# Performance work log

Measured on AMD Instinct MI355X. Metric: run time of the kernel, lower is better.

Reference implementation:

```python
import jax, jax.numpy as jnp
import numpy as np

B, T, EMB, H = 4, 2048, 1024, 16
S = EMB // H


def setup_inputs() -> dict:
    key = jax.random.key(0)
    ks = jax.random.split(key, 7)
    x = jax.random.normal(ks[0], (B, T, EMB), dtype=jnp.float32)
    pad_amounts = jax.random.randint(ks[1], (B,), 0, 512, dtype=jnp.int64)
    Wk = jax.random.normal(ks[2], (S, S), dtype=jnp.float32) * (1.0 / np.sqrt(S))
    Wq = jax.random.normal(ks[3], (S, S), dtype=jnp.float32) * (1.0 / np.sqrt(S))
    Wv = jax.random.normal(ks[4], (S, S), dtype=jnp.float32) * (1.0 / np.sqrt(S))
    Wu = jax.random.normal(ks[5], (EMB, EMB), dtype=jnp.float32) * (1.0 / np.sqrt(EMB))
    bu = jax.random.normal(ks[6], (EMB,), dtype=jnp.float32) * 0.01
    return {"x": x, "Wk": Wk, "Wq": Wq, "Wv": Wv, "Wu": Wu, "bu": bu,
            "pad_amounts": pad_amounts}


def reference(x, Wk, Wq, Wv, Wu, bu, pad_amounts):
    b, t, e = x.shape
    h = H
    s = e // h
    xh = x.reshape(b, t, h, s)
    # torch Linear: y = x @ W.T (no bias for k/q/v)
    keys = jnp.einsum('bths,os->btho', xh, Wk)
    queries = jnp.einsum('bths,os->btho', xh, Wq)
    values = jnp.einsum('bths,os->btho', xh, Wv)
    # (b,t,h,s) -> (b*h,t,s)
    keys = keys.transpose(0, 2, 1, 3).reshape(b * h, t, s)
    queries = queries.transpose(0, 2, 1, 3).reshape(b * h, t, s)
    values = values.transpose(0, 2, 1, 3).reshape(b * h, t, s)
    scale = e ** 0.25
    queries = queries / scale
    keys = keys / scale
    dot = jnp.einsum('nqs,nks->nqk', queries, keys)  # (b*h, t, t)
    # Faithful to original bug: only the first b flat indices of b*h get masked.
    pad_full = jnp.concatenate([pad_amounts,
                                jnp.zeros(b * h - b, dtype=pad_amounts.dtype)])
    thresh = (t - pad_full)[:, None, None]  # (b*h,1,1); thresh=t -> no mask
    pos = jnp.arange(t)
    mask = (pos[None, :, None] >= thresh) & (pos[None, None, :] >= thresh)
    dot = jnp.where(mask, -jnp.inf, dot)
    att = jax.nn.softmax(dot, axis=2)
    out = jnp.einsum('nqk,nks->nqs', att, values)  # (b*h,t,s)
    out = out.reshape(b, h, t, s).transpose(0, 2, 1, 3).reshape(b, t, h * s)
    return out @ Wu.T + bu
```

## Files before the change

### kernel.cpp

```cpp
#include <hip/hip_runtime.h>


typedef float f32x4 __attribute__((ext_vector_type(4)));
typedef float f32x16 __attribute__((ext_vector_type(16)));
typedef __bf16 bf16x8 __attribute__((ext_vector_type(8)));
typedef unsigned u32x4 __attribute__((ext_vector_type(4)));

#define MFMA16(a, b, c) __builtin_amdgcn_mfma_f32_16x16x32_bf16((a), (b), (c), 0, 0, 0)
#define MFMA32(a, b, c) __builtin_amdgcn_mfma_f32_32x32x16_bf16((a), (b), (c), 0, 0, 0)

constexpr int Tn = 2048;
constexpr int Bn = 4;
constexpr int EMBn = 1024;
constexpr float NEG_INF = -3.0e38f;

__device__ __forceinline__ float exp2_hw(float x) {
  float r; asm("v_exp_f32 %0, %1" : "=v"(r) : "v"(x)); return r;
}
__device__ __forceinline__ unsigned cvtpk(float lo, float hi) {
  unsigned r; asm("v_cvt_pk_bf16_f32 %0, %1, %2" : "=v"(r) : "v"(lo), "v"(hi)); return r;
}
__device__ __forceinline__ void permswap(unsigned& a, unsigned& b) {
  asm("v_permlane32_swap_b32 %0, %1" : "+v"(a), "+v"(b));
}

__global__ __launch_bounds__(256) void sa_prep(
    const float* __restrict__ Wk, const float* __restrict__ Wq,
    const float* __restrict__ Wv, const float* __restrict__ Wu,
    __bf16* __restrict__ w3, __bf16* __restrict__ wub) {
  int idx = blockIdx.x * 256 + threadIdx.x;
  const float rs = 0.21233046f;
  if (idx < 1048576) wub[idx] = (__bf16)Wu[idx];
  if (idx < 4096) {
    w3[idx]        = (__bf16)(Wk[idx] * rs);
    w3[4096 + idx] = (__bf16)(Wq[idx] * rs);
    w3[8192 + idx] = (__bf16)(Wv[idx]);
  }
}

__global__ __launch_bounds__(256) void sa_qkv(
    const float* __restrict__ x, const __bf16* __restrict__ w3,
    __bf16* __restrict__ Qb, __bf16* __restrict__ Kb, __bf16* __restrict__ Vt) {
  const int wave = threadIdx.x >> 6;
  const int lane = threadIdx.x & 63;
  const int g = lane >> 4, c = lane & 15;
  const int n = blockIdx.y, b = n >> 4, h = n & 15;
  const int t0 = blockIdx.x * 64 + wave * 16;

  bf16x8 ax[2];
#pragma unroll
  for (int kk = 0; kk < 2; ++kk) {
    const float* xp = x + ((long)((b * Tn + t0 + c) * 16 + h)) * 64 + kk * 32 + g * 8;
    f32x4 u = *(const f32x4*)xp;
    f32x4 v = *(const f32x4*)(xp + 4);
    bf16x8 a;
    a[0] = (__bf16)u[0]; a[1] = (__bf16)u[1]; a[2] = (__bf16)u[2]; a[3] = (__bf16)u[3];
    a[4] = (__bf16)v[0]; a[5] = (__bf16)v[1]; a[6] = (__bf16)v[2]; a[7] = (__bf16)v[3];
    ax[kk] = a;
  }

#pragma unroll
  for (int w = 0; w < 2; ++w) {
    __bf16* dst = w ? Qb : Kb;
#pragma unroll
    for (int ot = 0; ot < 4; ++ot) {
      f32x4 a_ = {0.f, 0.f, 0.f, 0.f};
#pragma unroll
      for (int kk = 0; kk < 2; ++kk) {
        bf16x8 wf = *(const bf16x8*)(w3 + w * 4096 + (ot * 16 + c) * 64 + kk * 32 + g * 8);
        a_ = MFMA16(ax[kk], wf, a_);
      }
#pragma unroll
      for (int r = 0; r < 4; ++r)
        dst[((long)n * Tn + t0 + g * 4 + r) * 64 + ot * 16 + c] = (__bf16)a_[r];
    }
  }

#pragma unroll
  for (int ot = 0; ot < 4; ++ot) {
    f32x4 a_ = {0.f, 0.f, 0.f, 0.f};
#pragma unroll
    for (int kk = 0; kk < 2; ++kk) {
      bf16x8 wf = *(const bf16x8*)(w3 + 8192 + (ot * 16 + c) * 64 + kk * 32 + g * 8);
      a_ = MFMA16(wf, ax[kk], a_);
    }
#pragma unroll
    for (int r = 0; r < 4; ++r)
      Vt[((long)n * 64 + ot * 16 + g * 4 + r) * Tn + t0 + c] = (__bf16)a_[r];
  }
}

__global__ __launch_bounds__(256, 4) void sa_flash(
    const __bf16* __restrict__ Qb, const __bf16* __restrict__ Kb,
    const __bf16* __restrict__ Vt, const int* __restrict__ pad32,
    __bf16* __restrict__ AO) {
  const int bid = blockIdx.x;
  const int n = (bid & 7) * 8 + (bid >> 7);
  const int qblk = (bid >> 3) & 15;
  const int tid = threadIdx.x;
  const int wave = tid >> 6;
  const int lane = tid & 63;
  const int ql = lane & 31;
  const int hi = lane >> 5;

  int thresh = Tn;
  if (n < Bn) {
    bool is64 = (pad32[1] == 0 && pad32[3] == 0);
    int pv = is64 ? pad32[2 * n] : pad32[n];
    thresh = Tn - pv;
  }

  const int qbase = qblk * 128 + wave * 32;
  const __bf16* Qh = Qb + (long)n * Tn * 64;
  const __bf16* Kh = Kb + (long)n * Tn * 64;
  const __bf16* Vh = Vt + (long)n * 64 * Tn;

  bf16x8 bq[4];
  const __bf16* qp = Qh + (long)(qbase + ql) * 64 + hi * 8;
#pragma unroll
  for (int ks = 0; ks < 4; ++ks) bq[ks] = *(const bf16x8*)(qp + ks * 16);

  __shared__ __align__(16) char smem[16384];

  const int kr = tid >> 3, kc = tid & 7;
  const int vs = tid >> 2, vc = tid & 3;
  const __bf16* kgp = Kh + kr * 64 + kc * 8;
  const __bf16* vgp = Vh + (long)vs * Tn + vc * 8;
  char* kw = smem + kr * 128 + ((kc * 16) ^ ((kr & 7) << 4));
  char* vw = smem + 8192 + vs * 64 + ((vc * 16) ^ (((vs >> 1) & 3) << 4));

  const int kswz = (ql & 7) << 4;
  const int vswz = ((ql >> 1) & 3) << 4;
  const char* krd = smem + ql * 128;
  const char* vrd = smem + 8192 + ql * 64;

  f32x16 o[2];
#pragma unroll
  for (int i = 0; i < 16; ++i) { o[0][i] = 0.f; o[1][i] = 0.f; }
  float l = 0.f;
  const bool qge = (qbase + ql) >= thresh;
  const bool qany = (qbase + 32) > thresh;

  {
    bf16x8 k0 = *(const bf16x8*)kgp;
    bf16x8 v0 = *(const bf16x8*)vgp;
    *(bf16x8*)kw = k0;
    *(bf16x8*)vw = v0;
  }
  __syncthreads();

  int cur = 0;
  for (int kb = 0; kb < Tn; kb += 32) {
    const int kbn = (kb + 32) & (Tn - 1);
    bf16x8 kst = *(const bf16x8*)(kgp + kbn * 64);
    bf16x8 vst = *(const bf16x8*)(vgp + kbn);

    const int kbase = cur * 4096;

    bf16x8 ka0 = *(const bf16x8*)(krd + kbase + ((0 + hi * 16) ^ kswz));
    bf16x8 ka1 = *(const bf16x8*)(krd + kbase + ((32 + hi * 16) ^ kswz));
    bf16x8 ka2 = *(const bf16x8*)(krd + kbase + ((64 + hi * 16) ^ kswz));
    bf16x8 ka3 = *(const bf16x8*)(krd + kbase + ((96 + hi * 16) ^ kswz));

    f32x16 st;
#pragma unroll
    for (int i = 0; i < 16; ++i) st[i] = 0.f;
    st = MFMA32(ka0, bq[0], st);
    st = MFMA32(ka1, bq[1], st);
    st = MFMA32(ka2, bq[2], st);
    st = MFMA32(ka3, bq[3], st);

    if (qany && (kb + 32) > thresh) {
      if (qge) {
#pragma unroll
        for (int r = 0; r < 16; ++r) {
          int kr_ = kb + (r & 3) + 8 * (r >> 2) + 4 * hi;
          if (kr_ >= thresh) st[r] = NEG_INF;
        }
      }
    }

    float p[16];
#pragma unroll
    for (int r = 0; r < 16; ++r) p[r] = exp2_hw(st[r]);
    float s8[8], s4[4];
#pragma unroll
    for (int i = 0; i < 8; ++i) s8[i] = p[i] + p[i + 8];
#pragma unroll
    for (int i = 0; i < 4; ++i) s4[i] = s8[i] + s8[i + 4];
    l += (s4[0] + s4[1]) + (s4[2] + s4[3]);

    unsigned pw[8];
#pragma unroll
    for (int j = 0; j < 2; ++j) {
      unsigned a0 = cvtpk(p[j * 8 + 0], p[j * 8 + 1]);
      unsigned b0 = cvtpk(p[j * 8 + 4], p[j * 8 + 5]);
      permswap(a0, b0);
      unsigned a1 = cvtpk(p[j * 8 + 2], p[j * 8 + 3]);
      unsigned b1 = cvtpk(p[j * 8 + 6], p[j * 8 + 7]);
      permswap(a1, b1);
      pw[j * 4 + 0] = a0; pw[j * 4 + 1] = a1;
      pw[j * 4 + 2] = b0; pw[j * 4 + 3] = b1;
    }
    u32x4 u0 = {pw[0], pw[1], pw[2], pw[3]};
    u32x4 u1 = {pw[4], pw[5], pw[6], pw[7]};
    bf16x8 pb0 = __builtin_bit_cast(bf16x8, u0);
    bf16x8 pb1 = __builtin_bit_cast(bf16x8, u1);

    bf16x8 va0 = *(const bf16x8*)(vrd + kbase + ((0 + hi * 16) ^ vswz));
    bf16x8 va1 = *(const bf16x8*)(vrd + kbase + ((32 + hi * 16) ^ vswz));
    bf16x8 va2 = *(const bf16x8*)(vrd + kbase + 2048 + ((0 + hi * 16) ^ vswz));
    bf16x8 va3 = *(const bf16x8*)(vrd + kbase + 2048 + ((32 + hi * 16) ^ vswz));

    o[0] = MFMA32(va0, pb0, o[0]);
    o[0] = MFMA32(va1, pb1, o[0]);
    o[1] = MFMA32(va2, pb0, o[1]);
    o[1] = MFMA32(va3, pb1, o[1]);

    *(bf16x8*)(kw + (cur ^ 1) * 4096) = kst;
    *(bf16x8*)(vw + (cur ^ 1) * 4096) = vst;
    __syncthreads();
    cur ^= 1;
  }

  float lf = l + __shfl_xor(l, 32, 64);
  float linv = 1.0f / lf;

  __bf16* my = (__bf16*)(smem + wave * 4096);
#pragma unroll
  for (int stile = 0; stile < 2; ++stile) {
#pragma unroll
    for (int r = 0; r < 16; r += 2) {
      unsigned wv = cvtpk(o[stile][r] * linv, o[stile][r + 1] * linv);
      int s = stile * 32 + (r & 3) + 8 * (r >> 2) + 4 * hi;
      *(unsigned*)(my + ql * 64 + (s ^ ((ql & 7) << 3))) = wv;
    }
  }
  asm volatile("s_waitcnt lgkmcnt(0)" ::: "memory");

  const int bb = n >> 4, hh = n & 15;
  const int qr = lane >> 3, s0 = (lane & 7) * 8;
#pragma unroll
  for (int j = 0; j < 4; ++j) {
    int q = j * 8 + qr;
    bf16x8 vv = *(const bf16x8*)(my + q * 64 + (s0 ^ ((q & 7) << 3)));
    *(bf16x8*)(AO + ((long)(bb * Tn + qbase + q)) * EMBn + hh * 64 + s0) = vv;
  }
}

__global__ __launch_bounds__(256, 4) void sa_oproj(
    const __bf16* __restrict__ A, const __bf16* __restrict__ WuB,
    const float* __restrict__ bu, float* __restrict__ Y) {
  const int bid = blockIdx.x;
  const int nstrip = (bid & 7) * 2 + ((bid >> 3) & 1);
  const int mblk = bid >> 4;
  const int tid = threadIdx.x;
  const int wave = tid >> 6;
  const int lane = tid & 63;
  const int ql = lane & 31;
  const int hi = lane >> 5;
  const int mbase = mblk * 128 + wave * 32;
  const int nbase = nstrip * 64;

  __shared__ __align__(16) char bsm[16384];
  const int sr = tid >> 3, sc = tid & 7;
  const __bf16* wg0 = WuB + (long)(nbase + sr) * 1024 + sc * 8;
  const __bf16* wg1 = WuB + (long)(nbase + sr + 32) * 1024 + sc * 8;
  const int wofs = ((sc * 16) ^ ((sr & 7) << 4));
  char* ww0 = bsm + sr * 128 + wofs;
  char* ww1 = bsm + (sr + 32) * 128 + wofs;

  const __bf16* ap = A + (long)(mbase + ql) * 1024 + hi * 8;

  f32x16 acc[2];
#pragma unroll
  for (int i = 0; i < 16; ++i) { acc[0][i] = 0.f; acc[1][i] = 0.f; }

  {
    bf16x8 w0 = *(const bf16x8*)wg0;
    bf16x8 w1 = *(const bf16x8*)wg1;
    *(bf16x8*)ww0 = w0;
    *(bf16x8*)ww1 = w1;
  }
  __syncthreads();

  int cur = 0;
  for (int kb = 0; kb < 1024; kb += 64) {
    const int kbn = (kb + 64) & 1023;
    bf16x8 wn0 = *(const bf16x8*)(wg0 + kbn);
    bf16x8 wn1 = *(const bf16x8*)(wg1 + kbn);

    bf16x8 af[4];
#pragma unroll
    for (int ks = 0; ks < 4; ++ks) af[ks] = *(const bf16x8*)(ap + kb + ks * 16);

    const char* bbase = bsm + cur * 8192;
#pragma unroll
    for (int nt = 0; nt < 2; ++nt) {
      const char* brow = bbase + (nt * 32 + ql) * 128;
#pragma unroll
      for (int ks = 0; ks < 4; ++ks) {
        bf16x8 bf = *(const bf16x8*)(brow + (((ks * 2 + hi) * 16) ^ ((ql & 7) << 4)));
        acc[nt] = MFMA32(af[ks], bf, acc[nt]);
      }
    }

    *(bf16x8*)(ww0 + (cur ^ 1) * 8192) = wn0;
    *(bf16x8*)(ww1 + (cur ^ 1) * 8192) = wn1;
    __syncthreads();
    cur ^= 1;
  }

#pragma unroll
  for (int nt = 0; nt < 2; ++nt) {
    float bias = bu[nbase + nt * 32 + ql];
#pragma unroll
    for (int r = 0; r < 16; ++r) {
      int mrow = mbase + (r & 3) + 8 * (r >> 2) + 4 * hi;
      Y[(long)mrow * 1024 + nbase + nt * 32 + ql] = acc[nt][r] + bias;
    }
  }
}

extern "C" void kernel_launch(void* const* d_in, const int* in_sizes, int n_in,
                              void* d_out, int out_size, void* d_ws, size_t ws_size,
                              hipStream_t stream) {
  const float* x  = (const float*)d_in[0];
  const float* Wk = (const float*)d_in[1];
  const float* Wq = (const float*)d_in[2];
  const float* Wv = (const float*)d_in[3];
  const float* Wu = (const float*)d_in[4];
  const float* bu = (const float*)d_in[5];
  const int* pad  = (const int*)d_in[6];
  float* Y = (float*)d_out;

  __bf16* ws  = (__bf16*)d_ws;
  __bf16* w3  = ws;
  __bf16* wub = ws + 16384;
  __bf16* Qb  = ws + 16384 + 1048576;
  __bf16* Kb  = Qb + 8388608;
  __bf16* Vt  = Kb + 8388608;
  __bf16* AO  = Vt + 8388608;

  sa_prep<<<4096, 256, 0, stream>>>(Wk, Wq, Wv, Wu, w3, wub);
  sa_qkv<<<dim3(32, 64), 256, 0, stream>>>(x, w3, Qb, Kb, Vt);
  sa_flash<<<dim3(1024), 256, 0, stream>>>(Qb, Kb, Vt, pad, AO);
  sa_oproj<<<dim3(1024), 256, 0, stream>>>(AO, wub, bu, Y);
}
```

Before: 157.5 us.

## Switch pipeline to fp16 MFMA, padded LDS layouts, MFMA row-sum, oproj remap

Converts all intermediate buffers and MFMA ops from bf16 to fp16, using round-toward-zero packed conversion for probabilities. The XOR-swizzled LDS layouts in the flash and output-projection kernels are replaced with padded row strides. The softmax denominator is now accumulated with an extra MFMA against a vector of ones instead of scalar adds and a cross-lane shuffle. The output projection block-to-tile mapping is also reordered so each XCD handles a contiguous range of M blocks. fp16 has a narrower range than bf16, and the unnormalised exp values with no max subtraction could overflow for large logits.

```diff
diff --git a/kernel.cpp b/kernel.cpp
--- a/kernel.cpp
+++ b/kernel.cpp
@@ -3,11 +3,11 @@
 
 typedef float f32x4 __attribute__((ext_vector_type(4)));
 typedef float f32x16 __attribute__((ext_vector_type(16)));
-typedef __bf16 bf16x8 __attribute__((ext_vector_type(8)));
+typedef _Float16 f16x8 __attribute__((ext_vector_type(8)));
 typedef unsigned u32x4 __attribute__((ext_vector_type(4)));
 
-#define MFMA16(a, b, c) __builtin_amdgcn_mfma_f32_16x16x32_bf16((a), (b), (c), 0, 0, 0)
-#define MFMA32(a, b, c) __builtin_amdgcn_mfma_f32_32x32x16_bf16((a), (b), (c), 0, 0, 0)
+#define MFMA16(a, b, c) __builtin_amdgcn_mfma_f32_16x16x32_f16((a), (b), (c), 0, 0, 0)
+#define MFMA32(a, b, c) __builtin_amdgcn_mfma_f32_32x32x16_f16((a), (b), (c), 0, 0, 0)
 
 constexpr int Tn = 2048;
 constexpr int Bn = 4;
@@ -17,8 +17,8 @@
 __device__ __forceinline__ float exp2_hw(float x) {
   float r; asm("v_exp_f32 %0, %1" : "=v"(r) : "v"(x)); return r;
 }
-__device__ __forceinline__ unsigned cvtpk(float lo, float hi) {
-  unsigned r; asm("v_cvt_pk_bf16_f32 %0, %1, %2" : "=v"(r) : "v"(lo), "v"(hi)); return r;
+__device__ __forceinline__ unsigned pkrtz(float lo, float hi) {
+  unsigned r; asm("v_cvt_pkrtz_f16_f32 %0, %1, %2" : "=v"(r) : "v"(lo), "v"(hi)); return r;
 }
 __device__ __forceinline__ void permswap(unsigned& a, unsigned& b) {
   asm("v_permlane32_swap_b32 %0, %1" : "+v"(a), "+v"(b));
@@ -27,52 +27,52 @@
 __global__ __launch_bounds__(256) void sa_prep(
     const float* __restrict__ Wk, const float* __restrict__ Wq,
     const float* __restrict__ Wv, const float* __restrict__ Wu,
-    __bf16* __restrict__ w3, __bf16* __restrict__ wub) {
+    _Float16* __restrict__ w3, _Float16* __restrict__ wub) {
   int idx = blockIdx.x * 256 + threadIdx.x;
   const float rs = 0.21233046f;
-  if (idx < 1048576) wub[idx] = (__bf16)Wu[idx];
+  if (idx < 1048576) wub[idx] = (_Float16)Wu[idx];
   if (idx < 4096) {
-    w3[idx]        = (__bf16)(Wk[idx] * rs);
-    w3[4096 + idx] = (__bf16)(Wq[idx] * rs);
-    w3[8192 + idx] = (__bf16)(Wv[idx]);
+    w3[idx]        = (_Float16)(Wk[idx] * rs);
+    w3[4096 + idx] = (_Float16)(Wq[idx] * rs);
+    w3[8192 + idx] = (_Float16)(Wv[idx]);
   }
 }
 
 __global__ __launch_bounds__(256) void sa_qkv(
-    const float* __restrict__ x, const __bf16* __restrict__ w3,
-    __bf16* __restrict__ Qb, __bf16* __restrict__ Kb, __bf16* __restrict__ Vt) {
+    const float* __restrict__ x, const _Float16* __restrict__ w3,
+    _Float16* __restrict__ Qb, _Float16* __restrict__ Kb, _Float16* __restrict__ Vt) {
   const int wave = threadIdx.x >> 6;
   const int lane = threadIdx.x & 63;
   const int g = lane >> 4, c = lane & 15;
   const int n = blockIdx.y, b = n >> 4, h = n & 15;
   const int t0 = blockIdx.x * 64 + wave * 16;
 
-  bf16x8 ax[2];
+  f16x8 ax[2];
 #pragma unroll
   for (int kk = 0; kk < 2; ++kk) {
     const float* xp = x + ((long)((b * Tn + t0 + c) * 16 + h)) * 64 + kk * 32 + g * 8;
     f32x4 u = *(const f32x4*)xp;
     f32x4 v = *(const f32x4*)(xp + 4);
-    bf16x8 a;
-    a[0] = (__bf16)u[0]; a[1] = (__bf16)u[1]; a[2] = (__bf16)u[2]; a[3] = (__bf16)u[3];
-    a[4] = (__bf16)v[0]; a[5] = (__bf16)v[1]; a[6] = (__bf16)v[2]; a[7] = (__bf16)v[3];
+    f16x8 a;
+    a[0] = (_Float16)u[0]; a[1] = (_Float16)u[1]; a[2] = (_Float16)u[2]; a[3] = (_Float16)u[3];
+    a[4] = (_Float16)v[0]; a[5] = (_Float16)v[1]; a[6] = (_Float16)v[2]; a[7] = (_Float16)v[3];
     ax[kk] = a;
   }
 
 #pragma unroll
   for (int w = 0; w < 2; ++w) {
-    __bf16* dst = w ? Qb : Kb;
+    _Float16* dst = w ? Qb : Kb;
 #pragma unroll
     for (int ot = 0; ot < 4; ++ot) {
       f32x4 a_ = {0.f, 0.f, 0.f, 0.f};
 #pragma unroll
       for (int kk = 0; kk < 2; ++kk) {
-        bf16x8 wf = *(const bf16x8*)(w3 + w * 4096 + (ot * 16 + c) * 64 + kk * 32 + g * 8);
+        f16x8 wf = *(const f16x8*)(w3 + w * 4096 + (ot * 16 + c) * 64 + kk * 32 + g * 8);
         a_ = MFMA16(ax[kk], wf, a_);
       }
 #pragma unroll
       for (int r = 0; r < 4; ++r)
-        dst[((long)n * Tn + t0 + g * 4 + r) * 64 + ot * 16 + c] = (__bf16)a_[r];
+        dst[((long)n * Tn + t0 + g * 4 + r) * 64 + ot * 16 + c] = (_Float16)a_[r];
     }
   }
 
@@ -81,19 +81,19 @@
     f32x4 a_ = {0.f, 0.f, 0.f, 0.f};
 #pragma unroll
     for (int kk = 0; kk < 2; ++kk) {
-      bf16x8 wf = *(const bf16x8*)(w3 + 8192 + (ot * 16 + c) * 64 + kk * 32 + g * 8);
+      f16x8 wf = *(const f16x8*)(w3 + 8192 + (ot * 16 + c) * 64 + kk * 32 + g * 8);
       a_ = MFMA16(wf, ax[kk], a_);
     }
 #pragma unroll
     for (int r = 0; r < 4; ++r)
-      Vt[((long)n * 64 + ot * 16 + g * 4 + r) * Tn + t0 + c] = (__bf16)a_[r];
+      Vt[((long)n * 64 + ot * 16 + g * 4 + r) * Tn + t0 + c] = (_Float16)a_[r];
   }
 }
 
 __global__ __launch_bounds__(256, 4) void sa_flash(
-    const __bf16* __restrict__ Qb, const __bf16* __restrict__ Kb,
-    const __bf16* __restrict__ Vt, const int* __restrict__ pad32,
-    __bf16* __restrict__ AO) {
+    const _Float16* __restrict__ Qb, const _Float16* __restrict__ Kb,
+    const _Float16* __restrict__ Vt, const int* __restrict__ pad32,
+    _Float16* __restrict__ AO) {
   const int bid = blockIdx.x;
   const int n = (bid & 7) * 8 + (bid >> 7);
   const int qblk = (bid >> 3) & 15;
@@ -111,56 +111,58 @@
   }
 
   const int qbase = qblk * 128 + wave * 32;
-  const __bf16* Qh = Qb + (long)n * Tn * 64;
-  const __bf16* Kh = Kb + (long)n * Tn * 64;
-  const __bf16* Vh = Vt + (long)n * 64 * Tn;
-
-  bf16x8 bq[4];
-  const __bf16* qp = Qh + (long)(qbase + ql) * 64 + hi * 8;
-#pragma unroll
-  for (int ks = 0; ks < 4; ++ks) bq[ks] = *(const bf16x8*)(qp + ks * 16);
-
-  __shared__ __align__(16) char smem[16384];
+  const _Float16* Qh = Qb + (long)n * Tn * 64;
+  const _Float16* Kh = Kb + (long)n * Tn * 64;
+  const _Float16* Vh = Vt + (long)n * 64 * Tn;
+
+  f16x8 bq[4];
+  const _Float16* qp = Qh + (long)(qbase + ql) * 64 + hi * 8;
+#pragma unroll
+  for (int ks = 0; ks < 4; ++ks) bq[ks] = *(const f16x8*)(qp + ks * 16);
+
+  __shared__ __align__(16) char smem[19456];
 
   const int kr = tid >> 3, kc = tid & 7;
   const int vs = tid >> 2, vc = tid & 3;
-  const __bf16* kgp = Kh + kr * 64 + kc * 8;
-  const __bf16* vgp = Vh + (long)vs * Tn + vc * 8;
-  char* kw = smem + kr * 128 + ((kc * 16) ^ ((kr & 7) << 4));
-  char* vw = smem + 8192 + vs * 64 + ((vc * 16) ^ (((vs >> 1) & 3) << 4));
-
-  const int kswz = (ql & 7) << 4;
-  const int vswz = ((ql >> 1) & 3) << 4;
-  const char* krd = smem + ql * 128;
-  const char* vrd = smem + 8192 + ql * 64;
-
-  f32x16 o[2];
-#pragma unroll
-  for (int i = 0; i < 16; ++i) { o[0][i] = 0.f; o[1][i] = 0.f; }
-  float l = 0.f;
+  const _Float16* kgp = Kh + kr * 64 + kc * 8;
+  const _Float16* vgp = Vh + (long)vs * Tn + vc * 8;
+  char* kw = smem + kr * 144 + kc * 16;
+  char* vw = smem + 9216 + vs * 80 + vc * 16;
+
+  const char* krd = smem + ql * 144;
+  const char* vrd = smem + 9216 + ql * 80;
+
+  f32x16 o[2], o2;
+#pragma unroll
+  for (int i = 0; i < 16; ++i) { o[0][i] = 0.f; o[1][i] = 0.f; o2[i] = 0.f; }
+  f16x8 aones;
+#pragma unroll
+  for (int i = 0; i < 8; ++i) aones[i] = (_Float16)1.0f;
+
   const bool qge = (qbase + ql) >= thresh;
   const bool qany = (qbase + 32) > thresh;
 
   {
-    bf16x8 k0 = *(const bf16x8*)kgp;
-    bf16x8 v0 = *(const bf16x8*)vgp;
-    *(bf16x8*)kw = k0;
-    *(bf16x8*)vw = v0;
+    f16x8 k0 = *(const f16x8*)kgp;
+    f16x8 v0 = *(const f16x8*)vgp;
+    *(f16x8*)kw = k0;
+    *(f16x8*)vw = v0;
   }
   __syncthreads();
 
   int cur = 0;
   for (int kb = 0; kb < Tn; kb += 32) {
     const int kbn = (kb + 32) & (Tn - 1);
-    bf16x8 kst = *(const bf16x8*)(kgp + kbn * 64);
-    bf16x8 vst = *(const bf16x8*)(vgp + kbn);
-
-    const int kbase = cur * 4096;
-
-    bf16x8 ka0 = *(const bf16x8*)(krd + kbase + ((0 + hi * 16) ^ kswz));
-    bf16x8 ka1 = *(const bf16x8*)(krd + kbase + ((32 + hi * 16) ^ kswz));
-    bf16x8 ka2 = *(const bf16x8*)(krd + kbase + ((64 + hi * 16) ^ kswz));
-    bf16x8 ka3 = *(const bf16x8*)(krd + kbase + ((96 + hi * 16) ^ kswz));
+    f16x8 kst = *(const f16x8*)(kgp + kbn * 64);
+    f16x8 vst = *(const f16x8*)(vgp + kbn);
+
+    const int kbb = cur * 4608;
+    const int vbb = cur * 5120;
+
+    f16x8 ka0 = *(const f16x8*)(krd + kbb + 0 + hi * 16);
+    f16x8 ka1 = *(const f16x8*)(krd + kbb + 32 + hi * 16);
+    f16x8 ka2 = *(const f16x8*)(krd + kbb + 64 + hi * 16);
+    f16x8 ka3 = *(const f16x8*)(krd + kbb + 96 + hi * 16);
 
     f32x16 st;
 #pragma unroll
@@ -183,55 +185,50 @@
     float p[16];
 #pragma unroll
     for (int r = 0; r < 16; ++r) p[r] = exp2_hw(st[r]);
-    float s8[8], s4[4];
-#pragma unroll
-    for (int i = 0; i < 8; ++i) s8[i] = p[i] + p[i + 8];
-#pragma unroll
-    for (int i = 0; i < 4; ++i) s4[i] = s8[i] + s8[i + 4];
-    l += (s4[0] + s4[1]) + (s4[2] + s4[3]);
 
     unsigned pw[8];
 #pragma unroll
     for (int j = 0; j < 2; ++j) {
-      unsigned a0 = cvtpk(p[j * 8 + 0], p[j * 8 + 1]);
-      unsigned b0 = cvtpk(p[j * 8 + 4], p[j * 8 + 5]);
+      unsigned a0 = pkrtz(p[j * 8 + 0], p[j * 8 + 1]);
+      unsigned b0 = pkrtz(p[j * 8 + 4], p[j * 8 + 5]);
       permswap(a0, b0);
-      unsigned a1 = cvtpk(p[j * 8 + 2], p[j * 8 + 3]);
-      unsigned b1 = cvtpk(p[j * 8 + 6], p[j * 8 + 7]);
+      unsigned a1 = pkrtz(p[j * 8 + 2], p[j * 8 + 3]);
+      unsigned b1 = pkrtz(p[j * 8 + 6], p[j * 8 + 7]);
       permswap(a1, b1);
       pw[j * 4 + 0] = a0; pw[j * 4 + 1] = a1;
       pw[j * 4 + 2] = b0; pw[j * 4 + 3] = b1;
     }
     u32x4 u0 = {pw[0], pw[1], pw[2], pw[3]};
     u32x4 u1 = {pw[4], pw[5], pw[6], pw[7]};
-    bf16x8 pb0 = __builtin_bit_cast(bf16x8, u0);
-    bf16x8 pb1 = __builtin_bit_cast(bf16x8, u1);
-
-    bf16x8 va0 = *(const bf16x8*)(vrd + kbase + ((0 + hi * 16) ^ vswz));
-    bf16x8 va1 = *(const bf16x8*)(vrd + kbase + ((32 + hi * 16) ^ vswz));
-    bf16x8 va2 = *(const bf16x8*)(vrd + kbase + 2048 + ((0 + hi * 16) ^ vswz));
-    bf16x8 va3 = *(const bf16x8*)(vrd + kbase + 2048 + ((32 + hi * 16) ^ vswz));
+    f16x8 pb0 = __builtin_bit_cast(f16x8, u0);
+    f16x8 pb1 = __builtin_bit_cast(f16x8, u1);
+
+    f16x8 va0 = *(const f16x8*)(vrd + vbb + 0 + hi * 16);
+    f16x8 va1 = *(const f16x8*)(vrd + vbb + 32 + hi * 16);
+    f16x8 va2 = *(const f16x8*)(vrd + vbb + 2560 + 0 + hi * 16);
+    f16x8 va3 = *(const f16x8*)(vrd + vbb + 2560 + 32 + hi * 16);
 
     o[0] = MFMA32(va0, pb0, o[0]);
     o[0] = MFMA32(va1, pb1, o[0]);
     o[1] = MFMA32(va2, pb0, o[1]);
     o[1] = MFMA32(va3, pb1, o[1]);
-
-    *(bf16x8*)(kw + (cur ^ 1) * 4096) = kst;
-    *(bf16x8*)(vw + (cur ^ 1) * 4096) = vst;
+    o2 = MFMA32(aones, pb0, o2);
+    o2 = MFMA32(aones, pb1, o2);
+
+    *(f16x8*)(kw + (cur ^ 1) * 4608) = kst;
+    *(f16x8*)(vw + (cur ^ 1) * 5120) = vst;
     __syncthreads();
     cur ^= 1;
   }
 
-  float lf = l + __shfl_xor(l, 32, 64);
-  float linv = 1.0f / lf;
-
-  __bf16* my = (__bf16*)(smem + wave * 4096);
+  float linv = 1.0f / o2[0];
+
+  _Float16* my = (_Float16*)(smem + wave * 4096);
 #pragma unroll
   for (int stile = 0; stile < 2; ++stile) {
 #pragma unroll
     for (int r = 0; r < 16; r += 2) {
-      unsigned wv = cvtpk(o[stile][r] * linv, o[stile][r + 1] * linv);
+      unsigned wv = pkrtz(o[stile][r] * linv, o[stile][r + 1] * linv);
       int s = stile * 32 + (r & 3) + 8 * (r >> 2) + 4 * hi;
       *(unsigned*)(my + ql * 64 + (s ^ ((ql & 7) << 3))) = wv;
     }
@@ -243,17 +240,19 @@
 #pragma unroll
   for (int j = 0; j < 4; ++j) {
     int q = j * 8 + qr;
-    bf16x8 vv = *(const bf16x8*)(my + q * 64 + (s0 ^ ((q & 7) << 3)));
-    *(bf16x8*)(AO + ((long)(bb * Tn + qbase + q)) * EMBn + hh * 64 + s0) = vv;
+    f16x8 vv = *(const f16x8*)(my + q * 64 + (s0 ^ ((q & 7) << 3)));
+    *(f16x8*)(AO + ((long)(bb * Tn + qbase + q)) * EMBn + hh * 64 + s0) = vv;
   }
 }
 
 __global__ __launch_bounds__(256, 4) void sa_oproj(
-    const __bf16* __restrict__ A, const __bf16* __restrict__ WuB,
+    const _Float16* __restrict__ A, const _Float16* __restrict__ WuB,
     const float* __restrict__ bu, float* __restrict__ Y) {
   const int bid = blockIdx.x;
-  const int nstrip = (bid & 7) * 2 + ((bid >> 3) & 1);
-  const int mblk = bid >> 4;
+  const int xcd = bid & 7;
+  const int j = bid >> 3;
+  const int nstrip = j & 15;
+  const int mblk = xcd * 8 + (j >> 4);
   const int tid = threadIdx.x;
   const int wave = tid >> 6;
   const int lane = tid & 63;
@@ -262,51 +261,50 @@
   const int mbase = mblk * 128 + wave * 32;
   const int nbase = nstrip * 64;
 
-  __shared__ __align__(16) char bsm[16384];
+  __shared__ __align__(16) char bsm[18432];
   const int sr = tid >> 3, sc = tid & 7;
-  const __bf16* wg0 = WuB + (long)(nbase + sr) * 1024 + sc * 8;
-  const __bf16* wg1 = WuB + (long)(nbase + sr + 32) * 1024 + sc * 8;
-  const int wofs = ((sc * 16) ^ ((sr & 7) << 4));
-  char* ww0 = bsm + sr * 128 + wofs;
-  char* ww1 = bsm + (sr + 32) * 128 + wofs;
-
-  const __bf16* ap = A + (long)(mbase + ql) * 1024 + hi * 8;
+  const _Float16* wg0 = WuB + (long)(nbase + sr) * 1024 + sc * 8;
+  const _Float16* wg1 = WuB + (long)(nbase + sr + 32) * 1024 + sc * 8;
+  char* ww0 = bsm + sr * 144 + sc * 16;
+  char* ww1 = bsm + (sr + 32) * 144 + sc * 16;
+
+  const _Float16* ap = A + (long)(mbase + ql) * 1024 + hi * 8;
 
   f32x16 acc[2];
 #pragma unroll
   for (int i = 0; i < 16; ++i) { acc[0][i] = 0.f; acc[1][i] = 0.f; }
 
   {
-    bf16x8 w0 = *(const bf16x8*)wg0;
-    bf16x8 w1 = *(const bf16x8*)wg1;
-    *(bf16x8*)ww0 = w0;
-    *(bf16x8*)ww1 = w1;
+    f16x8 w0 = *(const f16x8*)wg0;
+    f16x8 w1 = *(const f16x8*)wg1;
+    *(f16x8*)ww0 = w0;
+    *(f16x8*)ww1 = w1;
   }
   __syncthreads();
 
   int cur = 0;
   for (int kb = 0; kb < 1024; kb += 64) {
     const int kbn = (kb + 64) & 1023;
-    bf16x8 wn0 = *(const bf16x8*)(wg0 + kbn);
-    bf16x8 wn1 = *(const bf16x8*)(wg1 + kbn);
-
-    bf16x8 af[4];
-#pragma unroll
-    for (int ks = 0; ks < 4; ++ks) af[ks] = *(const bf16x8*)(ap + kb + ks * 16);
-
-    const char* bbase = bsm + cur * 8192;
+    f16x8 wn0 = *(const f16x8*)(wg0 + kbn);
+    f16x8 wn1 = *(const f16x8*)(wg1 + kbn);
+
+    f16x8 af[4];
+#pragma unroll
+    for (int ks = 0; ks < 4; ++ks) af[ks] = *(const f16x8*)(ap + kb + ks * 16);
+
+    const char* bbase = bsm + cur * 9216;
 #pragma unroll
     for (int nt = 0; nt < 2; ++nt) {
-      const char* brow = bbase + (nt * 32 + ql) * 128;
+      const char* brow = bbase + (nt * 32 + ql) * 144;
 #pragma unroll
       for (int ks = 0; ks < 4; ++ks) {
-        bf16x8 bf = *(const bf16x8*)(brow + (((ks * 2 + hi) * 16) ^ ((ql & 7) << 4)));
+        f16x8 bf = *(const f16x8*)(brow + (ks * 2 + hi) * 16);
         acc[nt] = MFMA32(af[ks], bf, acc[nt]);
       }
     }
 
-    *(bf16x8*)(ww0 + (cur ^ 1) * 8192) = wn0;
-    *(bf16x8*)(ww1 + (cur ^ 1) * 8192) = wn1;
+    *(f16x8*)(ww0 + (cur ^ 1) * 9216) = wn0;
+    *(f16x8*)(ww1 + (cur ^ 1) * 9216) = wn1;
     __syncthreads();
     cur ^= 1;
   }
@@ -334,13 +332,13 @@
   const int* pad  = (const int*)d_in[6];
   float* Y = (float*)d_out;
 
-  __bf16* ws  = (__bf16*)d_ws;
-  __bf16* w3  = ws;
-  __bf16* wub = ws + 16384;
-  __bf16* Qb  = ws + 16384 + 1048576;
-  __bf16* Kb  = Qb + 8388608;
-  __bf16* Vt  = Kb + 8388608;
-  __bf16* AO  = Vt + 8388608;
+  _Float16* ws  = (_Float16*)d_ws;
+  _Float16* w3  = ws;
+  _Float16* wub = ws + 16384;
+  _Float16* Qb  = ws + 16384 + 1048576;
+  _Float16* Kb  = Qb + 8388608;
+  _Float16* Vt  = Kb + 8388608;
+  _Float16* AO  = Vt + 8388608;
 
   sa_prep<<<4096, 256, 0, stream>>>(Wk, Wq, Wv, Wu, w3, wub);
   sa_qkv<<<dim3(32, 64), 256, 0, stream>>>(x, w3, Qb, Kb, Vt);
```

After: 158.8 us. About the same (+0.9%).
